# Kernel tuning notes

Hardware: AMD Instinct MI355X
Metric: run time of the kernel (lower is better)

The kernel has to match this reference:

```python
import jax, jax.numpy as jnp
import numpy as np

B, CI, CO = 2, 32, 32
NX, NY, NZ = 64, 64, 64
M1, M2, M3 = 8, 8, 8
ZH = NZ // 2 + 1


def _dft_mat(N, sign):
    # Dense DFT twiddle matrix W[k, n] = exp(sign * 2j*pi*k*n/N), complex64.
    a = jnp.arange(N)
    ph = (sign * 2.0) * jnp.pi * jnp.outer(a, a).astype(jnp.float32) / N
    return jnp.exp(1j * ph)


def setup_inputs() -> dict:
    key = jax.random.key(0)
    ks = jax.random.split(key, 9)
    scale = 1.0 / (CI * CO)
    x = jax.random.normal(ks[0], (B, CI, NX, NY, NZ), dtype=jnp.float32)
    wshape = (CI, CO, M1, M2, M3)
    names = ['w1r', 'w1i', 'w2r', 'w2i', 'w3r', 'w3i', 'w4r', 'w4i']
    out = {'x': x}
    for i, nm in enumerate(names):
        out[nm] = scale * jax.random.uniform(ks[i + 1], wshape, dtype=jnp.float32)
    return out


def _dht3(x):
    # Naive O(N^2)-per-axis 3D DFT via dense matmuls; return real part.
    Wx = _dft_mat(NX, -1)
    Wy = _dft_mat(NY, -1)
    Wz = _dft_mat(NZ, -1)
    y = x.astype(jnp.complex64)
    y = jnp.einsum('bcxyz,xa->bcayz', y, Wx)
    y = jnp.einsum('bcxyz,ya->bcxaz', y, Wy)
    y = jnp.einsum('bcxyz,za->bcxya', y, Wz)
    return y.real


def _idht3(X):
    # Inverse DFT via dense matmuls; rectangular (ZH -> NZ) on last axis.
    Wxi = _dft_mat(NX, +1) / NX
    Wyi = _dft_mat(NY, +1) / NY
    kz = jnp.arange(ZH)
    nz = jnp.arange(NZ)
    Wzi = jnp.exp(1j * (2.0 * jnp.pi * jnp.outer(kz, nz).astype(jnp.float32) / NZ)) / NZ
    y = jnp.einsum('bcxyz,xa->bcayz', X, Wxi)
    y = jnp.einsum('bcxyz,ya->bcxaz', y, Wyi)
    y = jnp.einsum('bcxyz,za->bcxya', y, Wzi)
    return y.real


def _mul(a, b):
    # compl_mul3d: contract over input channels in the mode block.
    return jnp.einsum('bixyz,ioxyz->boxyz', a, b)


def reference(x, w1r, w1i, w2r, w2i, w3r, w3i, w4r, w4i):
    w1 = w1r + 1j * w1i
    w2 = w2r + 1j * w2i
    w3 = w3r + 1j * w3i
    w4 = w4r + 1j * w4i

    xd = _dht3(x)  # [B, CI, NX, NY, NZ] real

    out = jnp.zeros((B, CO, NX, NY, ZH), dtype=jnp.complex64)
    out = out.at[:, :, :M1, :M2, :M3].set(_mul(xd[:, :, :M1, :M2, :M3], w1))
    out = out.at[:, :, NX - M1:, :M2, :M3].set(_mul(xd[:, :, NX - M1:, :M2, :M3], w2))
    out = out.at[:, :, :M1, NY - M2:, :M3].set(_mul(xd[:, :, :M1, NY - M2:, :M3], w3))
    out = out.at[:, :, NX - M1:, NY - M2:, :M3].set(_mul(xd[:, :, NX - M1:, NY - M2:, :M3], w4))

    return _idht3(out)  # [B, CO, NX, NY, NZ] real
```

## Files before the change

kernel.cpp:

```cpp
#include <hip/hip_runtime.h>

#define PI2_64 0.098174770424681038f


__global__ __launch_bounds__(256) void k_fwd_zy(const float* __restrict__ x,
                                                float* __restrict__ z2) {
  __shared__ __align__(16) float sp[64 * 65];
  __shared__ __align__(8) float2 Z[64 * 9];
  __shared__ float rc[64], rs[64];
  int tid = threadIdx.x;

  const float4* xg = (const float4*)(x + (long)blockIdx.x * 4096);
#pragma unroll
  for (int j = 0; j < 4; ++j) {
    int idx = j * 256 + tid;
    float4 v = xg[idx];
    int flat = idx << 2;
    int y = flat >> 6, z = flat & 63;
    float* d = &sp[y * 65 + z];
    d[0] = v.x; d[1] = v.y; d[2] = v.z; d[3] = v.w;
  }
  if (tid < 64) {
    float s, c; __sincosf(PI2_64 * (float)tid, &s, &c);
    rc[tid] = c; rs[tid] = s;
  }
  __syncthreads();

  {
    int y2 = tid >> 3, kz = tid & 7;
    const float* r0 = &sp[y2 * 65];
    const float* r1 = &sp[(y2 + 32) * 65];
    float a0r = 0, a0i = 0, a1r = 0, a1i = 0;
    int m = 0;
#pragma unroll 4
    for (int z = 0; z < 64; ++z) {
      float c = rc[m], s = rs[m];
      float x0 = r0[z], x1 = r1[z];
      a0r = fmaf(x0, c, a0r); a0i = fmaf(-x0, s, a0i);
      a1r = fmaf(x1, c, a1r); a1i = fmaf(-x1, s, a1i);
      m = (m + kz) & 63;
    }
    Z[y2 * 9 + kz] = make_float2(a0r, a0i);
    Z[(y2 + 32) * 9 + kz] = make_float2(a1r, a1i);
  }
  __syncthreads();

  float2* pb = (float2*)sp;
  {
    int kz = tid & 7, ky = (tid >> 3) & 15, h = tid >> 7;
    int f = (ky < 8) ? ky : (48 + ky);
    float ar = 0, ai = 0;
    int m = (h * 32 * f) & 63;
#pragma unroll 4
    for (int yy = h * 32; yy < h * 32 + 32; ++yy) {
      float2 zv = Z[yy * 9 + kz];
      float c = rc[m], s = rs[m];
      ar += zv.x * c + zv.y * s;
      ai += zv.y * c - zv.x * s;
      m = (m + f) & 63;
    }
    pb[ky * 9 + kz + 144 * h] = make_float2(ar, ai);
  }
  __syncthreads();
  if (tid < 128) {
    int kz = tid & 7, ky = tid >> 3;
    float2 a = pb[ky * 9 + kz], b = pb[ky * 9 + kz + 144];
    ((float2*)z2)[(long)blockIdx.x * 128 + tid] = make_float2(a.x + b.x, a.y + b.y);
  }
}

__global__ __launch_bounds__(128) void k_fwd_x(const float* __restrict__ z2,
                                               float* __restrict__ xc) {
  __shared__ __align__(16) float s[64 * 16];
  int tid = threadIdx.x;
  int bi = blockIdx.x >> 4;
  int u = blockIdx.x & 15;
  const float* src = z2 + (long)bi * 16384 + u * 16;
  {
    int xr = tid >> 1, c0 = (tid & 1) * 8;
    const float4* p = (const float4*)(src + xr * 256 + c0);
    float4* q = (float4*)(s + xr * 16 + c0);
    q[0] = p[0]; q[1] = p[1];
  }
  __syncthreads();
  int t = tid >> 3, v = tid & 7;
  int f = (t < 8) ? t : 48 + t;
  float bs, bc; __sincosf(-PI2_64 * (float)f, &bs, &bc);
  float wr = 1.f, wi = 0.f, acc = 0.f;
  for (int xx = 0; xx < 64; ++xx) {
    float zr = s[xx * 16 + v * 2], zi = s[xx * 16 + v * 2 + 1];
    acc += zr * wr - zi * wi;
    float nr = wr * bc - wi * bs;
    wi = wr * bs + wi * bc;
    wr = nr;
  }
  xc[(long)bi * 2048 + t * 128 + u * 8 + v] = acc;
}

__global__ __launch_bounds__(256) void k_mix(const float* __restrict__ xc,
    const float* __restrict__ w1r, const float* __restrict__ w1i,
    const float* __restrict__ w2r, const float* __restrict__ w2i,
    const float* __restrict__ w3r, const float* __restrict__ w3i,
    const float* __restrict__ w4r, const float* __restrict__ w4i,
    float* __restrict__ outm) {
  __shared__ float sx[256];
  int tid = threadIdx.x;
  int b = blockIdx.x >> 8;
  int t = (blockIdx.x >> 4) & 15;
  int u = blockIdx.x & 15;
  {
    int i = tid >> 3, v = tid & 7;
    sx[tid] = xc[(long)(b * 32 + i) * 2048 + t * 128 + u * 8 + v];
  }
  __syncthreads();
  const float* wr_ = (t < 8) ? ((u < 8) ? w1r : w3r) : ((u < 8) ? w2r : w4r);
  const float* wi_ = (t < 8) ? ((u < 8) ? w1i : w3i) : ((u < 8) ? w2i : w4i);
  int tm = t & 7, um = u & 7;
  int o = tid >> 3, v = tid & 7;
  long woff = (long)o * 512 + tm * 64 + um * 8 + v;
  float ar = 0.f, ai = 0.f;
#pragma unroll 4
  for (int i = 0; i < 32; ++i) {
    float xv = sx[i * 8 + v];
    ar = fmaf(xv, wr_[woff + (long)i * 16384], ar);
    ai = fmaf(xv, wi_[woff + (long)i * 16384], ai);
  }
  long oi = (long)(b * 32 + o) * 2048 + t * 128 + u * 8 + v;
  ((float2*)outm)[oi] = make_float2(ar, ai);
}

__global__ __launch_bounds__(256) void k_inv_xyz(const float* __restrict__ outm,
                                                 float* __restrict__ out) {
  __shared__ __align__(8) float2 P[16 * 16 * 9];
  __shared__ __align__(8) float2 Y2[64 * 9];
  __shared__ __align__(8) float2 Y1[16 * 9];
  __shared__ float rc[64], rs[64];
  int tid = threadIdx.x;
  int bo = blockIdx.x >> 6, xx = blockIdx.x & 63;

  const float2* pg = (const float2*)(outm + (long)bo * 4096);
#pragma unroll
  for (int j = 0; j < 8; ++j) {
    int k = j * 256 + tid;
    int v = k & 7, tu = k >> 3;
    P[tu * 9 + v] = pg[k];
  }
  if (tid < 64) {
    float s, c; __sincosf(PI2_64 * (float)tid, &s, &c);
    rc[tid] = c; rs[tid] = s;
  }
  __syncthreads();

  float2* pb = Y2;
  {
    int v = tid & 7, u = (tid >> 3) & 15, h = tid >> 7;
    float ar = 0, ai = 0;
#pragma unroll
    for (int t = h * 8; t < h * 8 + 8; ++t) {
      int f = (t < 8) ? t : (48 + t);
      int m = (f * xx) & 63;
      float2 p = P[(t * 16 + u) * 9 + v];
      float c = rc[m], s = rs[m];
      ar += p.x * c - p.y * s;
      ai += p.y * c + p.x * s;
    }
    pb[u * 9 + v + 144 * h] = make_float2(ar, ai);
  }
  __syncthreads();
  if (tid < 128) {
    int v = tid & 7, u = tid >> 3;
    float2 a = pb[u * 9 + v], b = pb[u * 9 + v + 144];
    Y1[u * 9 + v] = make_float2(a.x + b.x, a.y + b.y);
  }
  __syncthreads();

  {
    int v = tid & 7, y0 = tid >> 3;
    int ya = y0, yb = y0 + 32;
    float ar0 = 0, ai0 = 0, ar1 = 0, ai1 = 0;
#pragma unroll
    for (int u = 0; u < 16; ++u) {
      int f = (u < 8) ? u : (48 + u);
      float2 q = Y1[u * 9 + v];
      int ma = (f * ya) & 63, mb = (f * yb) & 63;
      float ca = rc[ma], sa = rs[ma];
      float cb = rc[mb], sb = rs[mb];
      ar0 += q.x * ca - q.y * sa; ai0 += q.y * ca + q.x * sa;
      ar1 += q.x * cb - q.y * sb; ai1 += q.y * cb + q.x * sb;
    }
    __syncthreads();
    Y2[ya * 9 + v] = make_float2(ar0, ai0);
    Y2[yb * 9 + v] = make_float2(ar1, ai1);
  }
  __syncthreads();

  {
    int zq = tid & 15, y0 = tid >> 4;
    int z0 = zq * 4;
    const float sc = 1.f / 262144.f;
    float acc[4][4] = {{0,0,0,0},{0,0,0,0},{0,0,0,0},{0,0,0,0}};
#pragma unroll
    for (int v = 0; v < 8; ++v) {
      int m0 = (v * z0) & 63, m1 = (m0 + v) & 63, m2 = (m1 + v) & 63, m3 = (m2 + v) & 63;
      float c0 = rc[m0], s0 = rs[m0], c1 = rc[m1], s1 = rs[m1];
      float c2 = rc[m2], s2 = rs[m2], c3 = rc[m3], s3 = rs[m3];
#pragma unroll
      for (int yo = 0; yo < 4; ++yo) {
        float2 q = Y2[(y0 + yo * 16) * 9 + v];
        acc[yo][0] += q.x * c0 - q.y * s0;
        acc[yo][1] += q.x * c1 - q.y * s1;
        acc[yo][2] += q.x * c2 - q.y * s2;
        acc[yo][3] += q.x * c3 - q.y * s3;
      }
    }
    float* ob = out + (long)blockIdx.x * 4096;
#pragma unroll
    for (int yo = 0; yo < 4; ++yo) {
      int y = y0 + yo * 16;
      ((float4*)(ob + y * 64 + z0))[0] =
          make_float4(acc[yo][0] * sc, acc[yo][1] * sc, acc[yo][2] * sc, acc[yo][3] * sc);
    }
  }
}

extern "C" void kernel_launch(void* const* d_in, const int* in_sizes, int n_in,
                              void* d_out, int out_size, void* d_ws, size_t ws_size,
                              hipStream_t stream) {
  (void)in_sizes; (void)n_in; (void)out_size; (void)ws_size;
  const float* x   = (const float*)d_in[0];
  const float* w1r = (const float*)d_in[1];
  const float* w1i = (const float*)d_in[2];
  const float* w2r = (const float*)d_in[3];
  const float* w2i = (const float*)d_in[4];
  const float* w3r = (const float*)d_in[5];
  const float* w3i = (const float*)d_in[6];
  const float* w4r = (const float*)d_in[7];
  const float* w4i = (const float*)d_in[8];
  float* out = (float*)d_out;
  float* ws = (float*)d_ws;

  float* z2   = ws;
  float* xc   = ws + 1048576;
  float* outm = ws + 1179648;

  k_fwd_zy <<<dim3(4096), dim3(256), 0, stream>>>(x, z2);
  k_fwd_x  <<<dim3(1024), dim3(128), 0, stream>>>(z2, xc);
  k_mix    <<<dim3(512),  dim3(256), 0, stream>>>(xc, w1r, w1i, w2r, w2i,
                                                  w3r, w3i, w4r, w4i, outm);
  k_inv_xyz<<<dim3(4096), dim3(256), 0, stream>>>(outm, out);
}
```

Measured before the change: 184.2 us.

## Exploit DFT even/odd symmetry in forward and inverse passes, widen mix per block

The forward z/y DFT now folds the input into even/odd pairs (x[p]±x[64-p]), so each cosine/sine twiddle is applied to half the samples, and reduces partial sums with wave shuffles. The inverse x and y stages apply the same symmetric folding. The z stage reads from a precomputed twiddle table held in shared memory. The mix kernel computes two u-columns per block, halving the grid and reusing loads. This removes redundant FLOPs and LDS traffic, at the cost of more shared memory, extra syncs and more complex indexing, which may reduce occupancy.

```diff
diff --git a/kernel.cpp b/kernel.cpp
--- a/kernel.cpp
+++ b/kernel.cpp
@@ -6,8 +6,9 @@
 __global__ __launch_bounds__(256) void k_fwd_zy(const float* __restrict__ x,
                                                 float* __restrict__ z2) {
   __shared__ __align__(16) float sp[64 * 65];
-  __shared__ __align__(8) float2 Z[64 * 9];
-  __shared__ float rc[64], rs[64];
+  __shared__ __align__(8) float2 Zc[64 * 9];
+  __shared__ __align__(8) float2 Ec[32 * 9], Oc[32 * 9];
+  __shared__ __align__(8) float2 cs[64];
   int tid = threadIdx.x;
 
   const float4* xg = (const float4*)(x + (long)blockIdx.x * 4096);
@@ -22,50 +23,91 @@
   }
   if (tid < 64) {
     float s, c; __sincosf(PI2_64 * (float)tid, &s, &c);
-    rc[tid] = c; rs[tid] = s;
-  }
-  __syncthreads();
-
-  {
-    int y2 = tid >> 3, kz = tid & 7;
-    const float* r0 = &sp[y2 * 65];
-    const float* r1 = &sp[(y2 + 32) * 65];
-    float a0r = 0, a0i = 0, a1r = 0, a1i = 0;
-    int m = 0;
-#pragma unroll 4
-    for (int z = 0; z < 64; ++z) {
-      float c = rc[m], s = rs[m];
-      float x0 = r0[z], x1 = r1[z];
-      a0r = fmaf(x0, c, a0r); a0i = fmaf(-x0, s, a0i);
-      a1r = fmaf(x1, c, a1r); a1i = fmaf(-x1, s, a1i);
-      m = (m + kz) & 63;
-    }
-    Z[y2 * 9 + kz] = make_float2(a0r, a0i);
-    Z[(y2 + 32) * 9 + kz] = make_float2(a1r, a1i);
-  }
-  __syncthreads();
-
-  float2* pb = (float2*)sp;
-  {
-    int kz = tid & 7, ky = (tid >> 3) & 15, h = tid >> 7;
-    int f = (ky < 8) ? ky : (48 + ky);
-    float ar = 0, ai = 0;
-    int m = (h * 32 * f) & 63;
-#pragma unroll 4
-    for (int yy = h * 32; yy < h * 32 + 32; ++yy) {
-      float2 zv = Z[yy * 9 + kz];
-      float c = rc[m], s = rs[m];
-      ar += zv.x * c + zv.y * s;
-      ai += zv.y * c - zv.x * s;
-      m = (m + f) & 63;
-    }
-    pb[ky * 9 + kz + 144 * h] = make_float2(ar, ai);
-  }
-  __syncthreads();
-  if (tid < 128) {
-    int kz = tid & 7, ky = tid >> 3;
-    float2 a = pb[ky * 9 + kz], b = pb[ky * 9 + kz + 144];
-    ((float2*)z2)[(long)blockIdx.x * 128 + tid] = make_float2(a.x + b.x, a.y + b.y);
+    cs[tid] = make_float2(c, s);
+  }
+  __syncthreads();
+
+  {
+    int y = tid >> 2, qp = tid & 3;
+    const float* row = &sp[y * 65];
+    float Sr[8] = {0,0,0,0,0,0,0,0}, So[8] = {0,0,0,0,0,0,0,0};
+    int p0 = qp * 8 + 1, pend = (qp == 3) ? 32 : (p0 + 8);
+    for (int p = p0; p < pend; ++p) {
+      float a = row[p], b = row[64 - p];
+      float e = a + b, o = a - b;
+      Sr[0] += e;
+      int m = p & 63;
+#pragma unroll
+      for (int k = 1; k < 8; ++k) {
+        float2 t = cs[m];
+        Sr[k] = fmaf(e, t.x, Sr[k]);
+        So[k] = fmaf(o, t.y, So[k]);
+        m = (m + p) & 63;
+      }
+    }
+    if (qp == 3) {
+      float x0 = row[0], x32 = row[32];
+      float a = x0 + x32, b = x0 - x32;
+#pragma unroll
+      for (int k = 0; k < 8; ++k) Sr[k] += (k & 1) ? b : a;
+    }
+#pragma unroll
+    for (int k = 0; k < 8; ++k) {
+      Sr[k] += __shfl_xor(Sr[k], 1); So[k] += __shfl_xor(So[k], 1);
+      Sr[k] += __shfl_xor(Sr[k], 2); So[k] += __shfl_xor(So[k], 2);
+    }
+    if (qp == 0) {
+#pragma unroll
+      for (int k = 0; k < 8; ++k) Zc[y * 9 + k] = make_float2(Sr[k], -So[k]);
+    }
+  }
+  __syncthreads();
+
+  if (tid < 248) {
+    int yp = (tid >> 3) + 1, k = tid & 7;
+    float2 a = Zc[yp * 9 + k], b = Zc[(64 - yp) * 9 + k];
+    Ec[yp * 9 + k] = make_float2(a.x + b.x, a.y + b.y);
+    Oc[yp * 9 + k] = make_float2(a.x - b.x, a.y - b.y);
+  }
+  __syncthreads();
+
+  {
+    int jp = tid >> 5, kz = (tid >> 2) & 7, h = tid & 3;
+    int j = jp + 1;
+    float S1 = 0, S2 = 0, S3 = 0, S4 = 0, S0r = 0, S0i = 0;
+    int p0 = h * 8 + 1, pend = (h == 3) ? 32 : (p0 + 8);
+    int m = (j * p0) & 63;
+    for (int yp = p0; yp < pend; ++yp) {
+      float2 E = Ec[yp * 9 + kz], O = Oc[yp * 9 + kz];
+      float2 t = cs[m];
+      S1 = fmaf(E.x, t.x, S1);
+      S2 = fmaf(O.y, t.y, S2);
+      S3 = fmaf(E.y, t.x, S3);
+      S4 = fmaf(O.x, t.y, S4);
+      if (jp == 7) { S0r += E.x; S0i += E.y; }
+      m = (m + j) & 63;
+    }
+    if (h == 3) {
+      float2 z0 = Zc[kz], z32 = Zc[32 * 9 + kz];
+      float sg = (j & 1) ? -1.f : 1.f;
+      S1 += z0.x + sg * z32.x;
+      S3 += z0.y + sg * z32.y;
+      if (jp == 7) { S0r += z0.x + z32.x; S0i += z0.y + z32.y; }
+    }
+    S1 += __shfl_xor(S1, 1); S1 += __shfl_xor(S1, 2);
+    S2 += __shfl_xor(S2, 1); S2 += __shfl_xor(S2, 2);
+    S3 += __shfl_xor(S3, 1); S3 += __shfl_xor(S3, 2);
+    S4 += __shfl_xor(S4, 1); S4 += __shfl_xor(S4, 2);
+    S0r += __shfl_xor(S0r, 1); S0r += __shfl_xor(S0r, 2);
+    S0i += __shfl_xor(S0i, 1); S0i += __shfl_xor(S0i, 2);
+    if (h == 0) {
+      float2* gz = (float2*)z2 + (long)blockIdx.x * 128;
+      float2 vA = (jp < 7) ? make_float2(S1 + S2, S3 - S4) : make_float2(S0r, S0i);
+      int tA = (jp < 7) ? j : 0;
+      float2 vB = make_float2(S1 - S2, S3 + S4);
+      gz[tA * 8 + kz] = vA;
+      gz[(16 - j) * 8 + kz] = vB;
+    }
   }
 }
 
@@ -103,123 +145,149 @@
     const float* __restrict__ w3r, const float* __restrict__ w3i,
     const float* __restrict__ w4r, const float* __restrict__ w4i,
     float* __restrict__ outm) {
-  __shared__ float sx[256];
+  __shared__ float sx[2 * 256];
   int tid = threadIdx.x;
-  int b = blockIdx.x >> 8;
-  int t = (blockIdx.x >> 4) & 15;
-  int u = blockIdx.x & 15;
+  int b = blockIdx.x >> 7;
+  int t = (blockIdx.x >> 3) & 15;
+  int uh = blockIdx.x & 7;
+  int u0 = uh * 2;
   {
     int i = tid >> 3, v = tid & 7;
-    sx[tid] = xc[(long)(b * 32 + i) * 2048 + t * 128 + u * 8 + v];
-  }
-  __syncthreads();
-  const float* wr_ = (t < 8) ? ((u < 8) ? w1r : w3r) : ((u < 8) ? w2r : w4r);
-  const float* wi_ = (t < 8) ? ((u < 8) ? w1i : w3i) : ((u < 8) ? w2i : w4i);
-  int tm = t & 7, um = u & 7;
+    long base = (long)(b * 32 + i) * 2048 + t * 128;
+    sx[tid]       = xc[base + u0 * 8 + v];
+    sx[256 + tid] = xc[base + (u0 + 1) * 8 + v];
+  }
+  __syncthreads();
+  const float* wr_ = (t < 8) ? ((u0 < 8) ? w1r : w3r) : ((u0 < 8) ? w2r : w4r);
+  const float* wi_ = (t < 8) ? ((u0 < 8) ? w1i : w3i) : ((u0 < 8) ? w2i : w4i);
+  int tm = t & 7, um0 = u0 & 7;
   int o = tid >> 3, v = tid & 7;
-  long woff = (long)o * 512 + tm * 64 + um * 8 + v;
-  float ar = 0.f, ai = 0.f;
+  long woff = (long)o * 512 + tm * 64 + um0 * 8 + v;
+  float ar0 = 0, ai0 = 0, ar1 = 0, ai1 = 0;
 #pragma unroll 4
   for (int i = 0; i < 32; ++i) {
-    float xv = sx[i * 8 + v];
-    ar = fmaf(xv, wr_[woff + (long)i * 16384], ar);
-    ai = fmaf(xv, wi_[woff + (long)i * 16384], ai);
-  }
-  long oi = (long)(b * 32 + o) * 2048 + t * 128 + u * 8 + v;
-  ((float2*)outm)[oi] = make_float2(ar, ai);
+    float x0 = sx[i * 8 + v], x1 = sx[256 + i * 8 + v];
+    long wo = woff + (long)i * 16384;
+    ar0 = fmaf(x0, wr_[wo], ar0);
+    ai0 = fmaf(x0, wi_[wo], ai0);
+    ar1 = fmaf(x1, wr_[wo + 8], ar1);
+    ai1 = fmaf(x1, wi_[wo + 8], ai1);
+  }
+  long oi = (long)(b * 32 + o) * 2048 + t * 128 + u0 * 8 + v;
+  ((float2*)outm)[oi] = make_float2(ar0, ai0);
+  ((float2*)outm)[oi + 8] = make_float2(ar1, ai1);
 }
 
 __global__ __launch_bounds__(256) void k_inv_xyz(const float* __restrict__ outm,
                                                  float* __restrict__ out) {
-  __shared__ __align__(8) float2 P[16 * 16 * 9];
-  __shared__ __align__(8) float2 Y2[64 * 9];
-  __shared__ __align__(8) float2 Y1[16 * 9];
+  __shared__ __align__(8) float2 E1[9 * 128], O1[9 * 128];
+  __shared__ __align__(16) float2 Y1c[128];
+  __shared__ __align__(16) float2 Y2c[64 * 10];
+  __shared__ __align__(8) float2 cs[64];
   __shared__ float rc[64], rs[64];
+  __shared__ __align__(16) float2 ct3[512];
   int tid = threadIdx.x;
   int bo = blockIdx.x >> 6, xx = blockIdx.x & 63;
 
-  const float2* pg = (const float2*)(outm + (long)bo * 4096);
-#pragma unroll
-  for (int j = 0; j < 8; ++j) {
-    int k = j * 256 + tid;
-    int v = k & 7, tu = k >> 3;
-    P[tu * 9 + v] = pg[k];
-  }
   if (tid < 64) {
     float s, c; __sincosf(PI2_64 * (float)tid, &s, &c);
-    rc[tid] = c; rs[tid] = s;
-  }
-  __syncthreads();
-
-  float2* pb = Y2;
-  {
-    int v = tid & 7, u = (tid >> 3) & 15, h = tid >> 7;
-    float ar = 0, ai = 0;
-#pragma unroll
-    for (int t = h * 8; t < h * 8 + 8; ++t) {
-      int f = (t < 8) ? t : (48 + t);
-      int m = (f * xx) & 63;
-      float2 p = P[(t * 16 + u) * 9 + v];
+    cs[tid] = make_float2(c, s); rc[tid] = c; rs[tid] = s;
+  }
+#pragma unroll
+  for (int it = 0; it < 2; ++it) {
+    int idx = tid + it * 256;
+    int zq = idx >> 7, rem = idx & 127, v = rem >> 4, i = rem & 15;
+    int m = (v * (zq * 16 + i)) & 63;
+    float s, c; __sincosf(PI2_64 * (float)m, &s, &c);
+    ct3[idx] = make_float2(c, s);
+  }
+  const float2* pg = (const float2*)outm + (long)bo * 2048;
+  for (int it = 0; it < 5; ++it) {
+    int idx = tid + it * 256;
+    if (idx < 1152) {
+      int j = idx >> 7, uv = idx & 127;
+      float2 pA = pg[j * 128 + uv];
+      float2 E, O;
+      if (j == 0)      { E = pA; O = make_float2(0.f, 0.f); }
+      else if (j == 8) { E = pA; O = make_float2(-pA.x, -pA.y); }
+      else {
+        float2 pB = pg[(16 - j) * 128 + uv];
+        E = make_float2(pA.x + pB.x, pA.y + pB.y);
+        O = make_float2(pA.x - pB.x, pA.y - pB.y);
+      }
+      E1[idx] = E; O1[idx] = O;
+    }
+  }
+  __syncthreads();
+
+  {
+    int u = tid >> 4, v = (tid >> 1) & 7, h = tid & 1;
+    int uv = u * 8 + v;
+    float Yr = 0, Yi = 0;
+    int j0 = h ? 5 : 0, j1 = h ? 9 : 5;
+    for (int j = j0; j < j1; ++j) {
+      float2 E = E1[(j << 7) + uv], O = O1[(j << 7) + uv];
+      float2 t = cs[(j * xx) & 63];
+      Yr += E.x * t.x - O.y * t.y;
+      Yi += E.y * t.x + O.x * t.y;
+    }
+    Yr += __shfl_xor(Yr, 1); Yi += __shfl_xor(Yi, 1);
+    if (h == 0) Y1c[uv] = make_float2(Yr, Yi);
+  }
+  __syncthreads();
+
+  {
+    int y = tid & 63, vq = tid >> 6, v0 = vq * 2;
+    float4 A0 = *(const float4*)(&Y1c[v0]);
+    float Yr0 = A0.x, Yi0 = A0.y, Yr1 = A0.z, Yi1 = A0.w;
+#pragma unroll
+    for (int j = 1; j < 8; ++j) {
+      float4 Aj = *(const float4*)(&Y1c[j * 8 + v0]);
+      float4 Bj = *(const float4*)(&Y1c[(16 - j) * 8 + v0]);
+      int m = (j * y) & 63;
       float c = rc[m], s = rs[m];
-      ar += p.x * c - p.y * s;
-      ai += p.y * c + p.x * s;
-    }
-    pb[u * 9 + v + 144 * h] = make_float2(ar, ai);
-  }
-  __syncthreads();
-  if (tid < 128) {
-    int v = tid & 7, u = tid >> 3;
-    float2 a = pb[u * 9 + v], b = pb[u * 9 + v + 144];
-    Y1[u * 9 + v] = make_float2(a.x + b.x, a.y + b.y);
-  }
-  __syncthreads();
-
-  {
-    int v = tid & 7, y0 = tid >> 3;
-    int ya = y0, yb = y0 + 32;
-    float ar0 = 0, ai0 = 0, ar1 = 0, ai1 = 0;
-#pragma unroll
-    for (int u = 0; u < 16; ++u) {
-      int f = (u < 8) ? u : (48 + u);
-      float2 q = Y1[u * 9 + v];
-      int ma = (f * ya) & 63, mb = (f * yb) & 63;
-      float ca = rc[ma], sa = rs[ma];
-      float cb = rc[mb], sb = rs[mb];
-      ar0 += q.x * ca - q.y * sa; ai0 += q.y * ca + q.x * sa;
-      ar1 += q.x * cb - q.y * sb; ai1 += q.y * cb + q.x * sb;
-    }
-    __syncthreads();
-    Y2[ya * 9 + v] = make_float2(ar0, ai0);
-    Y2[yb * 9 + v] = make_float2(ar1, ai1);
-  }
-  __syncthreads();
-
-  {
-    int zq = tid & 15, y0 = tid >> 4;
-    int z0 = zq * 4;
+      float E0r = Aj.x + Bj.x, E0i = Aj.y + Bj.y;
+      float O0r = Aj.x - Bj.x, O0i = Aj.y - Bj.y;
+      float E1r = Aj.z + Bj.z, E1i = Aj.w + Bj.w;
+      float O1r = Aj.z - Bj.z, O1i = Aj.w - Bj.w;
+      Yr0 += E0r * c - O0i * s; Yi0 += E0i * c + O0r * s;
+      Yr1 += E1r * c - O1i * s; Yi1 += E1i * c + O1r * s;
+    }
+    {
+      float4 Aj = *(const float4*)(&Y1c[64 + v0]);
+      int m = (y * 8) & 63;
+      float c = rc[m], s = rs[m];
+      Yr0 += Aj.x * c + Aj.y * s; Yi0 += Aj.y * c - Aj.x * s;
+      Yr1 += Aj.z * c + Aj.w * s; Yi1 += Aj.w * c - Aj.z * s;
+    }
     const float sc = 1.f / 262144.f;
-    float acc[4][4] = {{0,0,0,0},{0,0,0,0},{0,0,0,0},{0,0,0,0}};
+    *(float4*)(&Y2c[y * 10 + v0]) =
+        make_float4(Yr0 * sc, Yi0 * sc, Yr1 * sc, Yi1 * sc);
+  }
+  __syncthreads();
+
+  {
+    int y = tid & 63, zq = tid >> 6;
+    const float4* rowp = (const float4*)(&Y2c[y * 10]);
+    float4 r0 = rowp[0], r1 = rowp[1], r2 = rowp[2], r3 = rowp[3];
+    float Yr[8] = {r0.x, r0.z, r1.x, r1.z, r2.x, r2.z, r3.x, r3.z};
+    float Yi[8] = {r0.y, r0.w, r1.y, r1.w, r2.y, r2.w, r3.y, r3.w};
+    float acc[16];
+#pragma unroll
+    for (int i = 0; i < 16; ++i) acc[i] = 0.f;
 #pragma unroll
     for (int v = 0; v < 8; ++v) {
-      int m0 = (v * z0) & 63, m1 = (m0 + v) & 63, m2 = (m1 + v) & 63, m3 = (m2 + v) & 63;
-      float c0 = rc[m0], s0 = rs[m0], c1 = rc[m1], s1 = rs[m1];
-      float c2 = rc[m2], s2 = rs[m2], c3 = rc[m3], s3 = rs[m3];
-#pragma unroll
-      for (int yo = 0; yo < 4; ++yo) {
-        float2 q = Y2[(y0 + yo * 16) * 9 + v];
-        acc[yo][0] += q.x * c0 - q.y * s0;
-        acc[yo][1] += q.x * c1 - q.y * s1;
-        acc[yo][2] += q.x * c2 - q.y * s2;
-        acc[yo][3] += q.x * c3 - q.y * s3;
+      const float2* ct = &ct3[(zq * 8 + v) * 16];
+#pragma unroll
+      for (int i = 0; i < 16; ++i) {
+        float2 t = ct[i];
+        acc[i] = fmaf(Yr[v], t.x, fmaf(-Yi[v], t.y, acc[i]));
       }
     }
-    float* ob = out + (long)blockIdx.x * 4096;
-#pragma unroll
-    for (int yo = 0; yo < 4; ++yo) {
-      int y = y0 + yo * 16;
-      ((float4*)(ob + y * 64 + z0))[0] =
-          make_float4(acc[yo][0] * sc, acc[yo][1] * sc, acc[yo][2] * sc, acc[yo][3] * sc);
-    }
+    float* ob = out + (long)blockIdx.x * 4096 + y * 64 + zq * 16;
+#pragma unroll
+    for (int q = 0; q < 4; ++q)
+      ((float4*)ob)[q] = make_float4(acc[q*4], acc[q*4+1], acc[q*4+2], acc[q*4+3]);
   }
 }
 
@@ -245,7 +313,7 @@
 
   k_fwd_zy <<<dim3(4096), dim3(256), 0, stream>>>(x, z2);
   k_fwd_x  <<<dim3(1024), dim3(128), 0, stream>>>(z2, xc);
-  k_mix    <<<dim3(512),  dim3(256), 0, stream>>>(xc, w1r, w1i, w2r, w2i,
+  k_mix    <<<dim3(256),  dim3(256), 0, stream>>>(xc, w1r, w1i, w2r, w2i,
                                                   w3r, w3i, w4r, w4i, outm);
   k_inv_xyz<<<dim3(4096), dim3(256), 0, stream>>>(outm, out);
 }
```

Result: no change. 184.4 us (+0.1%).
